# Optimization experiments

Hardware: AMD Instinct MI355X
Metric: run time of the kernel (lower is better)

Reference implementation:

```python
import jax, jax.numpy as jnp
import numpy as np

V, K, C, F = 100000, 64, 3, 16
HID = [64, 64, 64]  # 'large' pca-net hidden widths (config.yaml stand-in)
EPS = 1e-4


def setup_inputs() -> dict:
    key = jax.random.key(0)
    ks = jax.random.split(key, 12)
    inp = {
        "coordinates": jax.random.normal(ks[0], (V, C), jnp.float32),
        "distsq": jax.random.uniform(ks[1], (V, K), jnp.float32),
        "features": jax.random.uniform(ks[2], (V, F), jnp.float32),
        "n_idxs": jax.random.randint(ks[3], (V, K), 0, V, jnp.int32),
    }
    dims = [C * C] + HID + [C * C]
    for i in range(len(dims) - 1):
        fan_in = dims[i]
        inp[f"W{i}"] = jax.random.normal(ks[4 + 2 * i], (dims[i], dims[i + 1]), jnp.float32) / np.sqrt(fan_in)
        inp[f"b{i}"] = jnp.zeros((dims[i + 1],), jnp.float32)
    return inp


def _neighbour_covariance(coordinates, distsq, features, n_idxs):
    # gather neighbour coords/features: [V,K,C], [V,K,F]
    nbc = jnp.take(coordinates, n_idxs, axis=0)
    nbf = jnp.take(features, n_idxs, axis=0)
    # per-neighbour per-feature weights, distsq pre-scaled by 10 in call()
    w = nbf * jnp.exp(-10.0 * distsq)[:, :, None]          # [V,K,F]
    wsum = jnp.sum(w, axis=1) + EPS                         # [V,F]
    mean = jnp.einsum("vkf,vkc->vfc", w, nbc) / wsum[:, :, None]  # [V,F,C]
    # E[x x^T] - mu mu^T (avoids materializing [V,K,F,C] centered diffs)
    m2 = jnp.einsum("vkf,vkc,vkd->vfcd", w, nbc, nbc) / wsum[:, :, None, None]
    cov = m2 - mean[:, :, :, None] * mean[:, :, None, :]    # [V,F,C,C]
    return cov, mean


def reference(coordinates, distsq, features, n_idxs,
              W0, b0, W1, b1, W2, b2, W3, b3):
    cov, mean = _neighbour_covariance(coordinates, distsq, features, n_idxs)
    x = cov.reshape(-1, C * C)                              # [V*F, C^2]
    # per-layer path: ELU on every layer, including the final one
    for Wl, bl in ((W0, b0), (W1, b1), (W2, b2), (W3, b3)):
        x = jax.nn.elu(x @ Wl + bl)
    return x.reshape(-1, F * C * C)                         # [V, F*C^2]
```

## Files before the change

kernel.cpp:

```cpp
#include <hip/hip_runtime.h>
#include <math.h>

#define NV 100000
#define NK 64
#define NF 16
#define EPS_W 1e-4f
#define WS_NEED ((size_t)NV * 16 * 32)

typedef __attribute__((ext_vector_type(8))) short bf16x8;
typedef __attribute__((ext_vector_type(4))) float f32x4;

__device__ __forceinline__ unsigned int f2bfu(float x) {
    union { float f; unsigned int u; } a; a.f = x;
    return (a.u + 0x7FFFu + ((a.u >> 16) & 1u)) >> 16;
}
__device__ __forceinline__ unsigned int packbf(float lo, float hi) {
    return f2bfu(lo) | (f2bfu(hi) << 16);
}
__device__ __forceinline__ float eluf(float x) {
    return x > 0.f ? x : __expf(x) - 1.f;
}

__launch_bounds__(256)
__global__ void cov_kernel(const float* __restrict__ coords,
                           const float* __restrict__ distsq,
                           const float* __restrict__ feats,
                           const int*   __restrict__ nidx,
                           unsigned char* __restrict__ ws)
{
    __shared__ float sEW[16][64];
    __shared__ int   sIX[16][64];
    const int tid = threadIdx.x;
    const int gv  = tid >> 4;
    const int f   = tid & 15;
    const int v   = blockIdx.x * 16 + gv;

    {
        const size_t base = (size_t)v * NK + 4 * f;
        float4 d4 = *(const float4*)(distsq + base);
        int4   i4 = *(const int4*)(nidx + base);
        sEW[gv][4*f+0] = __expf(-10.f * d4.x);
        sEW[gv][4*f+1] = __expf(-10.f * d4.y);
        sEW[gv][4*f+2] = __expf(-10.f * d4.z);
        sEW[gv][4*f+3] = __expf(-10.f * d4.w);
        sIX[gv][4*f+0] = i4.x; sIX[gv][4*f+1] = i4.y;
        sIX[gv][4*f+2] = i4.z; sIX[gv][4*f+3] = i4.w;
    }
    __syncthreads();

    float s = 0.f, m0=0.f,m1=0.f,m2=0.f;
    float q00=0.f,q01=0.f,q02=0.f,q11=0.f,q12=0.f,q22=0.f;

    #pragma unroll 4
    for (int k = 0; k < NK; ++k) {
        int   idx = sIX[gv][k];
        float ew  = sEW[gv][k];
        float w   = feats[(size_t)idx * NF + f] * ew;
        float x = coords[(size_t)idx*3+0];
        float y = coords[(size_t)idx*3+1];
        float z = coords[(size_t)idx*3+2];
        s += w;
        m0 = fmaf(w,x,m0); m1 = fmaf(w,y,m1); m2 = fmaf(w,z,m2);
        float wx=w*x, wy=w*y, wz=w*z;
        q00=fmaf(wx,x,q00); q01=fmaf(wx,y,q01); q02=fmaf(wx,z,q02);
        q11=fmaf(wy,y,q11); q12=fmaf(wy,z,q12); q22=fmaf(wz,z,q22);
    }
    float inv = 1.f / (s + EPS_W);
    float mu0=m0*inv, mu1=m1*inv, mu2=m2*inv;
    float c00=fmaf(-mu0,mu0,q00*inv);
    float c01=fmaf(-mu0,mu1,q01*inv);
    float c02=fmaf(-mu0,mu2,q02*inv);
    float c11=fmaf(-mu1,mu1,q11*inv);
    float c12=fmaf(-mu1,mu2,q12*inv);
    float c22=fmaf(-mu2,mu2,q22*inv);

    uint4 lo, hi;
    lo.x = packbf(c00, c01);
    lo.y = packbf(c02, c01);
    lo.z = packbf(c11, c12);
    lo.w = packbf(c02, c12);
    hi.x = packbf(c22, 1.0f);
    hi.y = 0u; hi.z = 0u; hi.w = 0u;

    uint4* dst = (uint4*)(ws + ((size_t)v * 16 + f) * 32);
    dst[0] = lo;
    dst[1] = hi;
}

__device__ __forceinline__ bf16x8 rdfrag(const short* hb, int c, int g, int kc) {
    int boff = ((kc << 6) + (g << 4)) ^ ((c & 7) << 4);
    return *(const bf16x8*)(hb + c * 64 + (boff >> 1));
}
__device__ __forceinline__ void wrH(short* hb, int c, int g, int t,
                                    unsigned int p01, unsigned int p23) {
    int boff = ((t << 5) + (g << 3)) ^ ((c & 7) << 4);
    uint2 val; val.x = p01; val.y = p23;
    *(uint2*)(hb + c * 64 + (boff >> 1)) = val;
}

__launch_bounds__(256, 2)
__global__ void mlp_kernel(const unsigned char* __restrict__ ws,
                           const float* __restrict__ W0, const float* __restrict__ b0,
                           const float* __restrict__ W1, const float* __restrict__ b1,
                           const float* __restrict__ W2, const float* __restrict__ b2,
                           const float* __restrict__ W3, const float* __restrict__ b3,
                           float* __restrict__ out)
{
    __shared__ __align__(16) short hbuf[4][16 * 64];
    const int tid  = threadIdx.x;
    const int wid  = tid >> 6;
    const int lane = tid & 63;
    const int c    = lane & 15;
    const int g    = lane >> 4;
    short* hb = &hbuf[wid][0];

    union U8 { short s[8]; bf16x8 v; };

    bf16x8 w0f[4], w1f[8], w2f[8], w3f[2];
    #pragma unroll
    for (int t = 0; t < 4; ++t) {
        U8 u;
        #pragma unroll
        for (int i = 0; i < 8; ++i) {
            int k = 8 * g + i;
            float val = 0.f;
            if (k < 9)       val = W0[k * 64 + 16 * t + c];
            else if (k == 9) val = b0[16 * t + c];
            u.s[i] = (short)f2bfu(val);
        }
        w0f[t] = u.v;
    }
    #pragma unroll
    for (int t = 0; t < 4; ++t) {
        #pragma unroll
        for (int kc = 0; kc < 2; ++kc) {
            U8 u1, u2;
            #pragma unroll
            for (int i = 0; i < 8; ++i) {
                int k = 32 * kc + 8 * g + i;
                u1.s[i] = (short)f2bfu(W1[k * 64 + 16 * t + c]);
                u2.s[i] = (short)f2bfu(W2[k * 64 + 16 * t + c]);
            }
            w1f[2 * t + kc] = u1.v;
            w2f[2 * t + kc] = u2.v;
        }
    }
    #pragma unroll
    for (int kc = 0; kc < 2; ++kc) {
        U8 u;
        #pragma unroll
        for (int i = 0; i < 8; ++i) {
            int k = 32 * kc + 8 * g + i;
            u.s[i] = (short)f2bfu(c < 9 ? W3[k * 9 + c] : 0.f);
        }
        w3f[kc] = u.v;
    }

    float b1v[16], b2v[16], b3v[4];
    #pragma unroll
    for (int t = 0; t < 4; ++t)
        #pragma unroll
        for (int r = 0; r < 4; ++r) {
            b1v[4*t+r] = b1[16*t + 4*g + r];
            b2v[4*t+r] = b2[16*t + 4*g + r];
        }
    #pragma unroll
    for (int r = 0; r < 4; ++r)
        b3v[r] = (4*g + r < 9) ? b3[4*g + r] : 0.f;

    const int stride = gridDim.x * 4;
    for (int t0 = blockIdx.x * 4 + wid; t0 < NV; t0 += stride) {
        f32x4 a[4];
        {
            union { uint4 q; bf16x8 v; } bin;
            bin.q = *(const uint4*)(ws + (size_t)t0 * 512 + (c << 5) + ((g & 1) << 4));
            #pragma unroll
            for (int t = 0; t < 4; ++t) {
                f32x4 z4 = {0.f, 0.f, 0.f, 0.f};
                a[t] = __builtin_amdgcn_mfma_f32_16x16x32_bf16(w0f[t], bin.v, z4, 0, 0, 0);
            }
            #pragma unroll
            for (int t = 0; t < 4; ++t)
                wrH(hb, c, g, t, packbf(eluf(a[t][0]), eluf(a[t][1])),
                                 packbf(eluf(a[t][2]), eluf(a[t][3])));
        }
        {
            bf16x8 h0 = rdfrag(hb, c, g, 0);
            bf16x8 h1 = rdfrag(hb, c, g, 1);
            #pragma unroll
            for (int t = 0; t < 4; ++t) {
                f32x4 acc = { b1v[4*t+0], b1v[4*t+1], b1v[4*t+2], b1v[4*t+3] };
                acc = __builtin_amdgcn_mfma_f32_16x16x32_bf16(w1f[2*t+0], h0, acc, 0, 0, 0);
                acc = __builtin_amdgcn_mfma_f32_16x16x32_bf16(w1f[2*t+1], h1, acc, 0, 0, 0);
                a[t] = acc;
            }
            #pragma unroll
            for (int t = 0; t < 4; ++t)
                wrH(hb, c, g, t, packbf(eluf(a[t][0]), eluf(a[t][1])),
                                 packbf(eluf(a[t][2]), eluf(a[t][3])));
        }
        {
            bf16x8 h0 = rdfrag(hb, c, g, 0);
            bf16x8 h1 = rdfrag(hb, c, g, 1);
            #pragma unroll
            for (int t = 0; t < 4; ++t) {
                f32x4 acc = { b2v[4*t+0], b2v[4*t+1], b2v[4*t+2], b2v[4*t+3] };
                acc = __builtin_amdgcn_mfma_f32_16x16x32_bf16(w2f[2*t+0], h0, acc, 0, 0, 0);
                acc = __builtin_amdgcn_mfma_f32_16x16x32_bf16(w2f[2*t+1], h1, acc, 0, 0, 0);
                a[t] = acc;
            }
            #pragma unroll
            for (int t = 0; t < 4; ++t)
                wrH(hb, c, g, t, packbf(eluf(a[t][0]), eluf(a[t][1])),
                                 packbf(eluf(a[t][2]), eluf(a[t][3])));
        }
        {
            bf16x8 h0 = rdfrag(hb, c, g, 0);
            bf16x8 h1 = rdfrag(hb, c, g, 1);
            f32x4 acc = { b3v[0], b3v[1], b3v[2], b3v[3] };
            acc = __builtin_amdgcn_mfma_f32_16x16x32_bf16(w3f[0], h0, acc, 0, 0, 0);
            acc = __builtin_amdgcn_mfma_f32_16x16x32_bf16(w3f[1], h1, acc, 0, 0, 0);
            float* op = out + (size_t)(t0 * 16 + c) * 9 + (g << 2);
            if (g < 2) {
                op[0] = eluf(acc[0]); op[1] = eluf(acc[1]);
                op[2] = eluf(acc[2]); op[3] = eluf(acc[3]);
            } else if (g == 2) {
                op[0] = eluf(acc[0]);
            }
        }
    }
}

__launch_bounds__(256, 2)
__global__ void fused_pca_mlp(const float* __restrict__ coords,
                              const float* __restrict__ distsq,
                              const float* __restrict__ feats,
                              const int*   __restrict__ nidx,
                              const float* __restrict__ W0, const float* __restrict__ b0,
                              const float* __restrict__ W1, const float* __restrict__ b1,
                              const float* __restrict__ W2, const float* __restrict__ b2,
                              const float* __restrict__ W3, const float* __restrict__ b3,
                              float* __restrict__ out)
{
    __shared__ __align__(16) float sW0t[64 * 9];
    __shared__ __align__(16) float sW1t[64 * 64];
    __shared__ __align__(16) float sW2t[64 * 64];
    __shared__ __align__(16) float sW3t[9 * 64];
    __shared__ float sB0[64], sB1[64], sB2[64], sB3[9];
    const int tid = threadIdx.x;
    for (int t = tid; t < 64 * 9; t += 256) { int j = t / 9, i = t - j * 9; sW0t[t] = W0[i * 64 + j]; }
    for (int t = tid; t < 64 * 64; t += 256) { int j = t >> 6, i = t & 63; sW1t[t] = W1[i * 64 + j]; }
    for (int t = tid; t < 64 * 64; t += 256) { int j = t >> 6, i = t & 63; sW2t[t] = W2[i * 64 + j]; }
    for (int t = tid; t < 9 * 64; t += 256) { int j = t >> 6, i = t & 63; sW3t[t] = W3[i * 9 + j]; }
    if (tid < 64) { sB0[tid] = b0[tid]; sB1[tid] = b1[tid]; sB2[tid] = b2[tid]; }
    if (tid < 9)  { sB3[tid] = b3[tid]; }
    __syncthreads();
    const int g = tid >> 4, f = tid & 15;
    const int v = blockIdx.x * 16 + g;
    if (v >= NV) return;
    const int* nix = nidx + (size_t)v * NK;
    const float* dsq = distsq + (size_t)v * NK;
    float s = 0.f, m0=0,m1=0,m2=0, q00=0,q01=0,q02=0,q11=0,q12=0,q22=0;
    #pragma unroll 4
    for (int k = 0; k < NK; ++k) {
        int idx = nix[k];
        float ew = __expf(-10.0f * dsq[k]);
        float w = feats[(size_t)idx * NF + f] * ew;
        float x = coords[(size_t)idx*3+0], y = coords[(size_t)idx*3+1], z = coords[(size_t)idx*3+2];
        s += w; m0 = fmaf(w,x,m0); m1 = fmaf(w,y,m1); m2 = fmaf(w,z,m2);
        float wx=w*x, wy=w*y, wz=w*z;
        q00=fmaf(wx,x,q00); q01=fmaf(wx,y,q01); q02=fmaf(wx,z,q02);
        q11=fmaf(wy,y,q11); q12=fmaf(wy,z,q12); q22=fmaf(wz,z,q22);
    }
    float inv = 1.0f/(s+EPS_W), mu0=m0*inv, mu1=m1*inv, mu2=m2*inv;
    float xr[9];
    xr[0]=fmaf(-mu0,mu0,q00*inv); xr[1]=fmaf(-mu0,mu1,q01*inv); xr[2]=fmaf(-mu0,mu2,q02*inv);
    xr[3]=xr[1]; xr[4]=fmaf(-mu1,mu1,q11*inv); xr[5]=fmaf(-mu1,mu2,q12*inv);
    xr[6]=xr[2]; xr[7]=xr[5]; xr[8]=fmaf(-mu2,mu2,q22*inv);
    float h[64], gg[64];
    #pragma unroll
    for (int j = 0; j < 64; ++j) {
        float aa = sB0[j]; const float* wr = sW0t + j * 9;
        #pragma unroll
        for (int i = 0; i < 9; ++i) aa = fmaf(xr[i], wr[i], aa);
        h[j] = eluf(aa);
    }
    #pragma unroll
    for (int j = 0; j < 64; ++j) {
        float aa = sB1[j]; const float4* wr = (const float4*)(sW1t + (j << 6));
        #pragma unroll
        for (int i4 = 0; i4 < 16; ++i4) { float4 wv = wr[i4];
            aa = fmaf(h[4*i4+0],wv.x,aa); aa = fmaf(h[4*i4+1],wv.y,aa);
            aa = fmaf(h[4*i4+2],wv.z,aa); aa = fmaf(h[4*i4+3],wv.w,aa); }
        gg[j] = eluf(aa);
    }
    #pragma unroll
    for (int j = 0; j < 64; ++j) {
        float aa = sB2[j]; const float4* wr = (const float4*)(sW2t + (j << 6));
        #pragma unroll
        for (int i4 = 0; i4 < 16; ++i4) { float4 wv = wr[i4];
            aa = fmaf(gg[4*i4+0],wv.x,aa); aa = fmaf(gg[4*i4+1],wv.y,aa);
            aa = fmaf(gg[4*i4+2],wv.z,aa); aa = fmaf(gg[4*i4+3],wv.w,aa); }
        h[j] = eluf(aa);
    }
    float o[9];
    #pragma unroll
    for (int j = 0; j < 9; ++j) {
        float aa = sB3[j]; const float4* wr = (const float4*)(sW3t + (j << 6));
        #pragma unroll
        for (int i4 = 0; i4 < 16; ++i4) { float4 wv = wr[i4];
            aa = fmaf(h[4*i4+0],wv.x,aa); aa = fmaf(h[4*i4+1],wv.y,aa);
            aa = fmaf(h[4*i4+2],wv.z,aa); aa = fmaf(h[4*i4+3],wv.w,aa); }
        o[j] = eluf(aa);
    }
    float* op = out + ((size_t)v * NF + f) * 9;
    #pragma unroll
    for (int j = 0; j < 9; ++j) op[j] = o[j];
}

extern "C" void kernel_launch(void* const* d_in, const int* in_sizes, int n_in,
                              void* d_out, int out_size, void* d_ws, size_t ws_size,
                              hipStream_t stream) {
    (void)in_sizes; (void)n_in; (void)out_size;
    const float* coords = (const float*)d_in[0];
    const float* distsq = (const float*)d_in[1];
    const float* feats  = (const float*)d_in[2];
    const int*   nidx   = (const int*)d_in[3];
    const float* W0 = (const float*)d_in[4];
    const float* b0 = (const float*)d_in[5];
    const float* W1 = (const float*)d_in[6];
    const float* b1 = (const float*)d_in[7];
    const float* W2 = (const float*)d_in[8];
    const float* b2 = (const float*)d_in[9];
    const float* W3 = (const float*)d_in[10];
    const float* b3 = (const float*)d_in[11];
    float* out = (float*)d_out;

    if (ws_size >= WS_NEED) {
        unsigned char* ws = (unsigned char*)d_ws;
        hipLaunchKernelGGL(cov_kernel, dim3(NV / 16), dim3(256), 0, stream,
                           coords, distsq, feats, nidx, ws);
        hipLaunchKernelGGL(mlp_kernel, dim3(1024), dim3(256), 0, stream,
                           ws, W0, b0, W1, b1, W2, b2, W3, b3, out);
    } else {
        hipLaunchKernelGGL(fused_pca_mlp, dim3(NV / 16), dim3(256), 0, stream,
                           coords, distsq, feats, nidx,
                           W0, b0, W1, b1, W2, b2, W3, b3, out);
    }
}
```

Before: 209.8 us.

## Fuse covariance gather and MFMA MLP into one persistent per-wave kernel

```diff
diff --git a/kernel.cpp b/kernel.cpp
--- a/kernel.cpp
+++ b/kernel.cpp
@@ -5,86 +5,20 @@
 #define NK 64
 #define NF 16
 #define EPS_W 1e-4f
-#define WS_NEED ((size_t)NV * 16 * 32)
+#define NGRP (NV / 4)
+#define GRID 625
 
 typedef __attribute__((ext_vector_type(8))) short bf16x8;
 typedef __attribute__((ext_vector_type(4))) float f32x4;
 
-__device__ __forceinline__ unsigned int f2bfu(float x) {
-    union { float f; unsigned int u; } a; a.f = x;
-    return (a.u + 0x7FFFu + ((a.u >> 16) & 1u)) >> 16;
-}
-__device__ __forceinline__ unsigned int packbf(float lo, float hi) {
-    return f2bfu(lo) | (f2bfu(hi) << 16);
+__device__ __forceinline__ unsigned short bfu(float x) {
+    return __builtin_bit_cast(unsigned short, (__bf16)x);
+}
+__device__ __forceinline__ unsigned int pk2(float lo, float hi) {
+    return (unsigned int)bfu(lo) | ((unsigned int)bfu(hi) << 16);
 }
 __device__ __forceinline__ float eluf(float x) {
     return x > 0.f ? x : __expf(x) - 1.f;
-}
-
-__launch_bounds__(256)
-__global__ void cov_kernel(const float* __restrict__ coords,
-                           const float* __restrict__ distsq,
-                           const float* __restrict__ feats,
-                           const int*   __restrict__ nidx,
-                           unsigned char* __restrict__ ws)
-{
-    __shared__ float sEW[16][64];
-    __shared__ int   sIX[16][64];
-    const int tid = threadIdx.x;
-    const int gv  = tid >> 4;
-    const int f   = tid & 15;
-    const int v   = blockIdx.x * 16 + gv;
-
-    {
-        const size_t base = (size_t)v * NK + 4 * f;
-        float4 d4 = *(const float4*)(distsq + base);
-        int4   i4 = *(const int4*)(nidx + base);
-        sEW[gv][4*f+0] = __expf(-10.f * d4.x);
-        sEW[gv][4*f+1] = __expf(-10.f * d4.y);
-        sEW[gv][4*f+2] = __expf(-10.f * d4.z);
-        sEW[gv][4*f+3] = __expf(-10.f * d4.w);
-        sIX[gv][4*f+0] = i4.x; sIX[gv][4*f+1] = i4.y;
-        sIX[gv][4*f+2] = i4.z; sIX[gv][4*f+3] = i4.w;
-    }
-    __syncthreads();
-
-    float s = 0.f, m0=0.f,m1=0.f,m2=0.f;
-    float q00=0.f,q01=0.f,q02=0.f,q11=0.f,q12=0.f,q22=0.f;
-
-    #pragma unroll 4
-    for (int k = 0; k < NK; ++k) {
-        int   idx = sIX[gv][k];
-        float ew  = sEW[gv][k];
-        float w   = feats[(size_t)idx * NF + f] * ew;
-        float x = coords[(size_t)idx*3+0];
-        float y = coords[(size_t)idx*3+1];
-        float z = coords[(size_t)idx*3+2];
-        s += w;
-        m0 = fmaf(w,x,m0); m1 = fmaf(w,y,m1); m2 = fmaf(w,z,m2);
-        float wx=w*x, wy=w*y, wz=w*z;
-        q00=fmaf(wx,x,q00); q01=fmaf(wx,y,q01); q02=fmaf(wx,z,q02);
-        q11=fmaf(wy,y,q11); q12=fmaf(wy,z,q12); q22=fmaf(wz,z,q22);
-    }
-    float inv = 1.f / (s + EPS_W);
-    float mu0=m0*inv, mu1=m1*inv, mu2=m2*inv;
-    float c00=fmaf(-mu0,mu0,q00*inv);
-    float c01=fmaf(-mu0,mu1,q01*inv);
-    float c02=fmaf(-mu0,mu2,q02*inv);
-    float c11=fmaf(-mu1,mu1,q11*inv);
-    float c12=fmaf(-mu1,mu2,q12*inv);
-    float c22=fmaf(-mu2,mu2,q22*inv);
-
-    uint4 lo, hi;
-    lo.x = packbf(c00, c01);
-    lo.y = packbf(c02, c01);
-    lo.z = packbf(c11, c12);
-    lo.w = packbf(c02, c12);
-    hi.x = packbf(c22, 1.0f);
-    hi.y = 0u; hi.z = 0u; hi.w = 0u;
-
-    uint4* dst = (uint4*)(ws + ((size_t)v * 16 + f) * 32);
-    dst[0] = lo;
-    dst[1] = hi;
 }
 
 __device__ __forceinline__ bf16x8 rdfrag(const short* hb, int c, int g, int kc) {
@@ -98,21 +32,29 @@
     *(uint2*)(hb + c * 64 + (boff >> 1)) = val;
 }
 
-__launch_bounds__(256, 2)
-__global__ void mlp_kernel(const unsigned char* __restrict__ ws,
-                           const float* __restrict__ W0, const float* __restrict__ b0,
-                           const float* __restrict__ W1, const float* __restrict__ b1,
-                           const float* __restrict__ W2, const float* __restrict__ b2,
-                           const float* __restrict__ W3, const float* __restrict__ b3,
-                           float* __restrict__ out)
+__launch_bounds__(256, 3)
+__global__ void fused_kernel(const float* __restrict__ coords,
+                             const float* __restrict__ distsq,
+                             const float* __restrict__ feats,
+                             const int*   __restrict__ nidx,
+                             const float* __restrict__ W0, const float* __restrict__ b0,
+                             const float* __restrict__ W1, const float* __restrict__ b1,
+                             const float* __restrict__ W2, const float* __restrict__ b2,
+                             const float* __restrict__ W3, const float* __restrict__ b3,
+                             float* __restrict__ out)
 {
+    __shared__ float sEW[4][4][64];
+    __shared__ int   sIX[4][4][64];
+    __shared__ __align__(16) short rowbuf[4][64 * 24];
     __shared__ __align__(16) short hbuf[4][16 * 64];
+
     const int tid  = threadIdx.x;
     const int wid  = tid >> 6;
     const int lane = tid & 63;
-    const int c    = lane & 15;
-    const int g    = lane >> 4;
+    const int c = lane & 15;
+    const int g = lane >> 4;
     short* hb = &hbuf[wid][0];
+    short* rb = &rowbuf[wid][0];
 
     union U8 { short s[8]; bf16x8 v; };
 
@@ -126,7 +68,7 @@
             float val = 0.f;
             if (k < 9)       val = W0[k * 64 + 16 * t + c];
             else if (k == 9) val = b0[16 * t + c];
-            u.s[i] = (short)f2bfu(val);
+            u.s[i] = (short)bfu(val);
         }
         w0f[t] = u.v;
     }
@@ -138,8 +80,8 @@
             #pragma unroll
             for (int i = 0; i < 8; ++i) {
                 int k = 32 * kc + 8 * g + i;
-                u1.s[i] = (short)f2bfu(W1[k * 64 + 16 * t + c]);
-                u2.s[i] = (short)f2bfu(W2[k * 64 + 16 * t + c]);
+                u1.s[i] = (short)bfu(W1[k * 64 + 16 * t + c]);
+                u2.s[i] = (short)bfu(W2[k * 64 + 16 * t + c]);
             }
             w1f[2 * t + kc] = u1.v;
             w2f[2 * t + kc] = u2.v;
@@ -151,7 +93,7 @@
         #pragma unroll
         for (int i = 0; i < 8; ++i) {
             int k = 32 * kc + 8 * g + i;
-            u.s[i] = (short)f2bfu(c < 9 ? W3[k * 9 + c] : 0.f);
+            u.s[i] = (short)bfu(c < 9 ? W3[k * 9 + c] : 0.f);
         }
         w3f[kc] = u.v;
     }
@@ -161,167 +103,136 @@
     for (int t = 0; t < 4; ++t)
         #pragma unroll
         for (int r = 0; r < 4; ++r) {
-            b1v[4*t+r] = b1[16*t + 4*g + r];
-            b2v[4*t+r] = b2[16*t + 4*g + r];
+            b1v[4 * t + r] = b1[16 * t + 4 * g + r];
+            b2v[4 * t + r] = b2[16 * t + 4 * g + r];
         }
     #pragma unroll
     for (int r = 0; r < 4; ++r)
-        b3v[r] = (4*g + r < 9) ? b3[4*g + r] : 0.f;
-
-    const int stride = gridDim.x * 4;
-    for (int t0 = blockIdx.x * 4 + wid; t0 < NV; t0 += stride) {
-        f32x4 a[4];
+        b3v[r] = (4 * g + r < 9) ? b3[4 * g + r] : 0.f;
+
+    for (int grp = blockIdx.x * 4 + wid; grp < NGRP; grp += GRID * 4) {
+        const int v = grp * 4 + g;
+
         {
-            union { uint4 q; bf16x8 v; } bin;
-            bin.q = *(const uint4*)(ws + (size_t)t0 * 512 + (c << 5) + ((g & 1) << 4));
-            #pragma unroll
-            for (int t = 0; t < 4; ++t) {
-                f32x4 z4 = {0.f, 0.f, 0.f, 0.f};
-                a[t] = __builtin_amdgcn_mfma_f32_16x16x32_bf16(w0f[t], bin.v, z4, 0, 0, 0);
-            }
-            #pragma unroll
-            for (int t = 0; t < 4; ++t)
-                wrH(hb, c, g, t, packbf(eluf(a[t][0]), eluf(a[t][1])),
-                                 packbf(eluf(a[t][2]), eluf(a[t][3])));
-        }
+            const size_t base = (size_t)v * NK + 4 * c;
+            float4 d4 = *(const float4*)(distsq + base);
+            int4   i4 = *(const int4*)(nidx + base);
+            sEW[wid][g][4 * c + 0] = __expf(-10.f * d4.x);
+            sEW[wid][g][4 * c + 1] = __expf(-10.f * d4.y);
+            sEW[wid][g][4 * c + 2] = __expf(-10.f * d4.z);
+            sEW[wid][g][4 * c + 3] = __expf(-10.f * d4.w);
+            sIX[wid][g][4 * c + 0] = i4.x; sIX[wid][g][4 * c + 1] = i4.y;
+            sIX[wid][g][4 * c + 2] = i4.z; sIX[wid][g][4 * c + 3] = i4.w;
+        }
+        __asm__ volatile("s_waitcnt lgkmcnt(0)" ::: "memory");
+
+        float s = 0.f, m0 = 0.f, m1 = 0.f, m2 = 0.f;
+        float q00 = 0.f, q01 = 0.f, q02 = 0.f, q11 = 0.f, q12 = 0.f, q22 = 0.f;
+        #pragma unroll 4
+        for (int k = 0; k < NK; ++k) {
+            int   idx = sIX[wid][g][k];
+            float ew  = sEW[wid][g][k];
+            float w   = feats[(size_t)idx * NF + c] * ew;
+            float x = coords[(size_t)idx * 3 + 0];
+            float y = coords[(size_t)idx * 3 + 1];
+            float z = coords[(size_t)idx * 3 + 2];
+            s += w;
+            m0 = fmaf(w, x, m0); m1 = fmaf(w, y, m1); m2 = fmaf(w, z, m2);
+            float wx = w * x, wy = w * y, wz = w * z;
+            q00 = fmaf(wx, x, q00); q01 = fmaf(wx, y, q01); q02 = fmaf(wx, z, q02);
+            q11 = fmaf(wy, y, q11); q12 = fmaf(wy, z, q12);
+            q22 = fmaf(wz, z, q22);
+        }
+        float inv = 1.f / (s + EPS_W);
+        float mu0 = m0 * inv, mu1 = m1 * inv, mu2 = m2 * inv;
+        float c00 = fmaf(-mu0, mu0, q00 * inv);
+        float c01 = fmaf(-mu0, mu1, q01 * inv);
+        float c02 = fmaf(-mu0, mu2, q02 * inv);
+        float c11 = fmaf(-mu1, mu1, q11 * inv);
+        float c12 = fmaf(-mu1, mu2, q12 * inv);
+        float c22 = fmaf(-mu2, mu2, q22 * inv);
+
         {
-            bf16x8 h0 = rdfrag(hb, c, g, 0);
-            bf16x8 h1 = rdfrag(hb, c, g, 1);
-            #pragma unroll
-            for (int t = 0; t < 4; ++t) {
-                f32x4 acc = { b1v[4*t+0], b1v[4*t+1], b1v[4*t+2], b1v[4*t+3] };
-                acc = __builtin_amdgcn_mfma_f32_16x16x32_bf16(w1f[2*t+0], h0, acc, 0, 0, 0);
-                acc = __builtin_amdgcn_mfma_f32_16x16x32_bf16(w1f[2*t+1], h1, acc, 0, 0, 0);
-                a[t] = acc;
-            }
-            #pragma unroll
-            for (int t = 0; t < 4; ++t)
-                wrH(hb, c, g, t, packbf(eluf(a[t][0]), eluf(a[t][1])),
-                                 packbf(eluf(a[t][2]), eluf(a[t][3])));
-        }
-        {
-            bf16x8 h0 = rdfrag(hb, c, g, 0);
-            bf16x8 h1 = rdfrag(hb, c, g, 1);
-            #pragma unroll
-            for (int t = 0; t < 4; ++t) {
-                f32x4 acc = { b2v[4*t+0], b2v[4*t+1], b2v[4*t+2], b2v[4*t+3] };
-                acc = __builtin_amdgcn_mfma_f32_16x16x32_bf16(w2f[2*t+0], h0, acc, 0, 0, 0);
-                acc = __builtin_amdgcn_mfma_f32_16x16x32_bf16(w2f[2*t+1], h1, acc, 0, 0, 0);
-                a[t] = acc;
-            }
-            #pragma unroll
-            for (int t = 0; t < 4; ++t)
-                wrH(hb, c, g, t, packbf(eluf(a[t][0]), eluf(a[t][1])),
-                                 packbf(eluf(a[t][2]), eluf(a[t][3])));
-        }
-        {
-            bf16x8 h0 = rdfrag(hb, c, g, 0);
-            bf16x8 h1 = rdfrag(hb, c, g, 1);
-            f32x4 acc = { b3v[0], b3v[1], b3v[2], b3v[3] };
-            acc = __builtin_amdgcn_mfma_f32_16x16x32_bf16(w3f[0], h0, acc, 0, 0, 0);
-            acc = __builtin_amdgcn_mfma_f32_16x16x32_bf16(w3f[1], h1, acc, 0, 0, 0);
-            float* op = out + (size_t)(t0 * 16 + c) * 9 + (g << 2);
-            if (g < 2) {
-                op[0] = eluf(acc[0]); op[1] = eluf(acc[1]);
-                op[2] = eluf(acc[2]); op[3] = eluf(acc[3]);
-            } else if (g == 2) {
-                op[0] = eluf(acc[0]);
-            }
-        }
-    }
-}
-
-__launch_bounds__(256, 2)
-__global__ void fused_pca_mlp(const float* __restrict__ coords,
-                              const float* __restrict__ distsq,
-                              const float* __restrict__ feats,
-                              const int*   __restrict__ nidx,
-                              const float* __restrict__ W0, const float* __restrict__ b0,
-                              const float* __restrict__ W1, const float* __restrict__ b1,
-                              const float* __restrict__ W2, const float* __restrict__ b2,
-                              const float* __restrict__ W3, const float* __restrict__ b3,
-                              float* __restrict__ out)
-{
-    __shared__ __align__(16) float sW0t[64 * 9];
-    __shared__ __align__(16) float sW1t[64 * 64];
-    __shared__ __align__(16) float sW2t[64 * 64];
-    __shared__ __align__(16) float sW3t[9 * 64];
-    __shared__ float sB0[64], sB1[64], sB2[64], sB3[9];
-    const int tid = threadIdx.x;
-    for (int t = tid; t < 64 * 9; t += 256) { int j = t / 9, i = t - j * 9; sW0t[t] = W0[i * 64 + j]; }
-    for (int t = tid; t < 64 * 64; t += 256) { int j = t >> 6, i = t & 63; sW1t[t] = W1[i * 64 + j]; }
-    for (int t = tid; t < 64 * 64; t += 256) { int j = t >> 6, i = t & 63; sW2t[t] = W2[i * 64 + j]; }
-    for (int t = tid; t < 9 * 64; t += 256) { int j = t >> 6, i = t & 63; sW3t[t] = W3[i * 9 + j]; }
-    if (tid < 64) { sB0[tid] = b0[tid]; sB1[tid] = b1[tid]; sB2[tid] = b2[tid]; }
-    if (tid < 9)  { sB3[tid] = b3[tid]; }
-    __syncthreads();
-    const int g = tid >> 4, f = tid & 15;
-    const int v = blockIdx.x * 16 + g;
-    if (v >= NV) return;
-    const int* nix = nidx + (size_t)v * NK;
-    const float* dsq = distsq + (size_t)v * NK;
-    float s = 0.f, m0=0,m1=0,m2=0, q00=0,q01=0,q02=0,q11=0,q12=0,q22=0;
-    #pragma unroll 4
-    for (int k = 0; k < NK; ++k) {
-        int idx = nix[k];
-        float ew = __expf(-10.0f * dsq[k]);
-        float w = feats[(size_t)idx * NF + f] * ew;
-        float x = coords[(size_t)idx*3+0], y = coords[(size_t)idx*3+1], z = coords[(size_t)idx*3+2];
-        s += w; m0 = fmaf(w,x,m0); m1 = fmaf(w,y,m1); m2 = fmaf(w,z,m2);
-        float wx=w*x, wy=w*y, wz=w*z;
-        q00=fmaf(wx,x,q00); q01=fmaf(wx,y,q01); q02=fmaf(wx,z,q02);
-        q11=fmaf(wy,y,q11); q12=fmaf(wy,z,q12); q22=fmaf(wz,z,q22);
-    }
-    float inv = 1.0f/(s+EPS_W), mu0=m0*inv, mu1=m1*inv, mu2=m2*inv;
-    float xr[9];
-    xr[0]=fmaf(-mu0,mu0,q00*inv); xr[1]=fmaf(-mu0,mu1,q01*inv); xr[2]=fmaf(-mu0,mu2,q02*inv);
-    xr[3]=xr[1]; xr[4]=fmaf(-mu1,mu1,q11*inv); xr[5]=fmaf(-mu1,mu2,q12*inv);
-    xr[6]=xr[2]; xr[7]=xr[5]; xr[8]=fmaf(-mu2,mu2,q22*inv);
-    float h[64], gg[64];
-    #pragma unroll
-    for (int j = 0; j < 64; ++j) {
-        float aa = sB0[j]; const float* wr = sW0t + j * 9;
-        #pragma unroll
-        for (int i = 0; i < 9; ++i) aa = fmaf(xr[i], wr[i], aa);
-        h[j] = eluf(aa);
-    }
-    #pragma unroll
-    for (int j = 0; j < 64; ++j) {
-        float aa = sB1[j]; const float4* wr = (const float4*)(sW1t + (j << 6));
-        #pragma unroll
-        for (int i4 = 0; i4 < 16; ++i4) { float4 wv = wr[i4];
-            aa = fmaf(h[4*i4+0],wv.x,aa); aa = fmaf(h[4*i4+1],wv.y,aa);
-            aa = fmaf(h[4*i4+2],wv.z,aa); aa = fmaf(h[4*i4+3],wv.w,aa); }
-        gg[j] = eluf(aa);
-    }
-    #pragma unroll
-    for (int j = 0; j < 64; ++j) {
-        float aa = sB2[j]; const float4* wr = (const float4*)(sW2t + (j << 6));
-        #pragma unroll
-        for (int i4 = 0; i4 < 16; ++i4) { float4 wv = wr[i4];
-            aa = fmaf(gg[4*i4+0],wv.x,aa); aa = fmaf(gg[4*i4+1],wv.y,aa);
-            aa = fmaf(gg[4*i4+2],wv.z,aa); aa = fmaf(gg[4*i4+3],wv.w,aa); }
-        h[j] = eluf(aa);
-    }
-    float o[9];
-    #pragma unroll
-    for (int j = 0; j < 9; ++j) {
-        float aa = sB3[j]; const float4* wr = (const float4*)(sW3t + (j << 6));
-        #pragma unroll
-        for (int i4 = 0; i4 < 16; ++i4) { float4 wv = wr[i4];
-            aa = fmaf(h[4*i4+0],wv.x,aa); aa = fmaf(h[4*i4+1],wv.y,aa);
-            aa = fmaf(h[4*i4+2],wv.z,aa); aa = fmaf(h[4*i4+3],wv.w,aa); }
-        o[j] = eluf(aa);
-    }
-    float* op = out + ((size_t)v * NF + f) * 9;
-    #pragma unroll
-    for (int j = 0; j < 9; ++j) op[j] = o[j];
+            uint4 lo, hi;
+            lo.x = pk2(c00, c01);
+            lo.y = pk2(c02, c01);
+            lo.z = pk2(c11, c12);
+            lo.w = pk2(c02, c12);
+            hi.x = pk2(c22, 1.0f);
+            hi.y = 0u; hi.z = 0u; hi.w = 0u;
+            uint4* dst = (uint4*)(rb + lane * 24);
+            dst[0] = lo;
+            dst[1] = hi;
+        }
+        __asm__ volatile("s_waitcnt lgkmcnt(0)" ::: "memory");
+
+        #pragma unroll 1
+        for (int vv = 0; vv < 4; ++vv) {
+            f32x4 a[4];
+            {
+                bf16x8 bin = *(const bf16x8*)(rb + (16 * vv + c) * 24 + ((g & 1) << 3));
+                #pragma unroll
+                for (int t = 0; t < 4; ++t) {
+                    f32x4 z4 = {0.f, 0.f, 0.f, 0.f};
+                    a[t] = __builtin_amdgcn_mfma_f32_16x16x32_bf16(w0f[t], bin, z4, 0, 0, 0);
+                }
+                #pragma unroll
+                for (int t = 0; t < 4; ++t)
+                    wrH(hb, c, g, t, pk2(eluf(a[t][0]), eluf(a[t][1])),
+                                     pk2(eluf(a[t][2]), eluf(a[t][3])));
+            }
+            {
+                bf16x8 h0 = rdfrag(hb, c, g, 0);
+                bf16x8 h1 = rdfrag(hb, c, g, 1);
+                #pragma unroll
+                for (int t = 0; t < 4; ++t) {
+                    f32x4 acc = { b1v[4*t+0], b1v[4*t+1], b1v[4*t+2], b1v[4*t+3] };
+                    acc = __builtin_amdgcn_mfma_f32_16x16x32_bf16(w1f[2*t+0], h0, acc, 0, 0, 0);
+                    acc = __builtin_amdgcn_mfma_f32_16x16x32_bf16(w1f[2*t+1], h1, acc, 0, 0, 0);
+                    a[t] = acc;
+                }
+                #pragma unroll
+                for (int t = 0; t < 4; ++t)
+                    wrH(hb, c, g, t, pk2(eluf(a[t][0]), eluf(a[t][1])),
+                                     pk2(eluf(a[t][2]), eluf(a[t][3])));
+            }
+            {
+                bf16x8 h0 = rdfrag(hb, c, g, 0);
+                bf16x8 h1 = rdfrag(hb, c, g, 1);
+                #pragma unroll
+                for (int t = 0; t < 4; ++t) {
+                    f32x4 acc = { b2v[4*t+0], b2v[4*t+1], b2v[4*t+2], b2v[4*t+3] };
+                    acc = __builtin_amdgcn_mfma_f32_16x16x32_bf16(w2f[2*t+0], h0, acc, 0, 0, 0);
+                    acc = __builtin_amdgcn_mfma_f32_16x16x32_bf16(w2f[2*t+1], h1, acc, 0, 0, 0);
+                    a[t] = acc;
+                }
+                #pragma unroll
+                for (int t = 0; t < 4; ++t)
+                    wrH(hb, c, g, t, pk2(eluf(a[t][0]), eluf(a[t][1])),
+                                     pk2(eluf(a[t][2]), eluf(a[t][3])));
+            }
+            {
+                bf16x8 h0 = rdfrag(hb, c, g, 0);
+                bf16x8 h1 = rdfrag(hb, c, g, 1);
+                f32x4 acc = { b3v[0], b3v[1], b3v[2], b3v[3] };
+                acc = __builtin_amdgcn_mfma_f32_16x16x32_bf16(w3f[0], h0, acc, 0, 0, 0);
+                acc = __builtin_amdgcn_mfma_f32_16x16x32_bf16(w3f[1], h1, acc, 0, 0, 0);
+                float* op = out + (size_t)((grp * 4 + vv) * 16 + c) * 9 + (g << 2);
+                if (g < 2) {
+                    op[0] = eluf(acc[0]); op[1] = eluf(acc[1]);
+                    op[2] = eluf(acc[2]); op[3] = eluf(acc[3]);
+                } else if (g == 2) {
+                    op[0] = eluf(acc[0]);
+                }
+            }
+        }
+    }
 }
 
 extern "C" void kernel_launch(void* const* d_in, const int* in_sizes, int n_in,
                               void* d_out, int out_size, void* d_ws, size_t ws_size,
                               hipStream_t stream) {
-    (void)in_sizes; (void)n_in; (void)out_size;
+    (void)in_sizes; (void)n_in; (void)out_size; (void)d_ws; (void)ws_size;
     const float* coords = (const float*)d_in[0];
     const float* distsq = (const float*)d_in[1];
     const float* feats  = (const float*)d_in[2];
@@ -336,15 +247,7 @@
     const float* b3 = (const float*)d_in[11];
     float* out = (float*)d_out;
 
-    if (ws_size >= WS_NEED) {
-        unsigned char* ws = (unsigned char*)d_ws;
-        hipLaunchKernelGGL(cov_kernel, dim3(NV / 16), dim3(256), 0, stream,
-                           coords, distsq, feats, nidx, ws);
-        hipLaunchKernelGGL(mlp_kernel, dim3(1024), dim3(256), 0, stream,
-                           ws, W0, b0, W1, b1, W2, b2, W3, b3, out);
-    } else {
-        hipLaunchKernelGGL(fused_pca_mlp, dim3(NV / 16), dim3(256), 0, stream,
-                           coords, distsq, feats, nidx,
-                           W0, b0, W1, b1, W2, b2, W3, b3, out);
-    }
-}
+    hipLaunchKernelGGL(fused_kernel, dim3(GRID), dim3(256), 0, stream,
+                       coords, distsq, feats, nidx,
+                       W0, b0, W1, b1, W2, b2, W3, b3, out);
+}
```

After: 341.5 us. 62.8% more time.

## Precompute per-neighbour coordinate moments in shared memory, reducing covariance to feature dot products

Applied to the files above, without the earlier changes.

```diff
diff --git a/kernel.cpp b/kernel.cpp
--- a/kernel.cpp
+++ b/kernel.cpp
@@ -6,80 +6,87 @@
 #define NF 16
 #define EPS_W 1e-4f
 #define WS_NEED ((size_t)NV * 16 * 32)
+#define ZSTRIDE 776
 
 typedef __attribute__((ext_vector_type(8))) short bf16x8;
 typedef __attribute__((ext_vector_type(4))) float f32x4;
 
-__device__ __forceinline__ unsigned int f2bfu(float x) {
-    union { float f; unsigned int u; } a; a.f = x;
-    return (a.u + 0x7FFFu + ((a.u >> 16) & 1u)) >> 16;
-}
-__device__ __forceinline__ unsigned int packbf(float lo, float hi) {
-    return f2bfu(lo) | (f2bfu(hi) << 16);
+__device__ __forceinline__ unsigned short bfu(float x) {
+    return __builtin_bit_cast(unsigned short, (__bf16)x);
+}
+__device__ __forceinline__ unsigned int pk2(float lo, float hi) {
+    return (unsigned int)bfu(lo) | ((unsigned int)bfu(hi) << 16);
 }
 __device__ __forceinline__ float eluf(float x) {
     return x > 0.f ? x : __expf(x) - 1.f;
 }
 
 __launch_bounds__(256)
-__global__ void cov_kernel(const float* __restrict__ coords,
-                           const float* __restrict__ distsq,
-                           const float* __restrict__ feats,
-                           const int*   __restrict__ nidx,
-                           unsigned char* __restrict__ ws)
+__global__ void cov2_kernel(const float* __restrict__ coords,
+                            const float* __restrict__ distsq,
+                            const float* __restrict__ feats,
+                            const int*   __restrict__ nidx,
+                            unsigned char* __restrict__ ws)
 {
-    __shared__ float sEW[16][64];
-    __shared__ int   sIX[16][64];
+    __shared__ __align__(16) float sZ[16 * ZSTRIDE];
+
     const int tid = threadIdx.x;
-    const int gv  = tid >> 4;
-    const int f   = tid & 15;
-    const int v   = blockIdx.x * 16 + gv;
-
-    {
-        const size_t base = (size_t)v * NK + 4 * f;
-        float4 d4 = *(const float4*)(distsq + base);
-        int4   i4 = *(const int4*)(nidx + base);
-        sEW[gv][4*f+0] = __expf(-10.f * d4.x);
-        sEW[gv][4*f+1] = __expf(-10.f * d4.y);
-        sEW[gv][4*f+2] = __expf(-10.f * d4.z);
-        sEW[gv][4*f+3] = __expf(-10.f * d4.w);
-        sIX[gv][4*f+0] = i4.x; sIX[gv][4*f+1] = i4.y;
-        sIX[gv][4*f+2] = i4.z; sIX[gv][4*f+3] = i4.w;
+
+    #pragma unroll
+    for (int r = 0; r < 4; ++r) {
+        int t  = tid + r * 256;
+        int gv = t >> 6, k = t & 63;
+        int v  = blockIdx.x * 16 + gv;
+        float d  = distsq[(size_t)v * NK + k];
+        int  idx = nidx[(size_t)v * NK + k];
+        float ew = __expf(-10.f * d);
+        const float* cp = coords + (size_t)idx * 3;
+        float x = cp[0], y = cp[1], z = cp[2];
+        float* zr = sZ + gv * ZSTRIDE + k * 12;
+        float4 z0 = { ew * x * x, ew * x * y, ew * x * z, ew * y * y };
+        float4 z1 = { ew * y * z, ew * z * z, ew * x,     ew * y     };
+        float4 z2 = { ew * z,     ew,         __int_as_float(idx), 0.f };
+        *(float4*)(zr + 0) = z0;
+        *(float4*)(zr + 4) = z1;
+        *(float4*)(zr + 8) = z2;
     }
     __syncthreads();
 
-    float s = 0.f, m0=0.f,m1=0.f,m2=0.f;
-    float q00=0.f,q01=0.f,q02=0.f,q11=0.f,q12=0.f,q22=0.f;
+    const int gv = tid >> 4, f = tid & 15;
+    const int v  = blockIdx.x * 16 + gv;
+    const float* zb = sZ + gv * ZSTRIDE;
+
+    float a0=0.f,a1=0.f,a2=0.f,a3=0.f,a4=0.f,a5=0.f,a6=0.f,a7=0.f,a8=0.f,a9=0.f;
 
     #pragma unroll 4
     for (int k = 0; k < NK; ++k) {
-        int   idx = sIX[gv][k];
-        float ew  = sEW[gv][k];
-        float w   = feats[(size_t)idx * NF + f] * ew;
-        float x = coords[(size_t)idx*3+0];
-        float y = coords[(size_t)idx*3+1];
-        float z = coords[(size_t)idx*3+2];
-        s += w;
-        m0 = fmaf(w,x,m0); m1 = fmaf(w,y,m1); m2 = fmaf(w,z,m2);
-        float wx=w*x, wy=w*y, wz=w*z;
-        q00=fmaf(wx,x,q00); q01=fmaf(wx,y,q01); q02=fmaf(wx,z,q02);
-        q11=fmaf(wy,y,q11); q12=fmaf(wy,z,q12); q22=fmaf(wz,z,q22);
-    }
-    float inv = 1.f / (s + EPS_W);
-    float mu0=m0*inv, mu1=m1*inv, mu2=m2*inv;
-    float c00=fmaf(-mu0,mu0,q00*inv);
-    float c01=fmaf(-mu0,mu1,q01*inv);
-    float c02=fmaf(-mu0,mu2,q02*inv);
-    float c11=fmaf(-mu1,mu1,q11*inv);
-    float c12=fmaf(-mu1,mu2,q12*inv);
-    float c22=fmaf(-mu2,mu2,q22*inv);
+        float4 z0 = *(const float4*)(zb + k * 12 + 0);
+        float4 z1 = *(const float4*)(zb + k * 12 + 4);
+        float4 z2 = *(const float4*)(zb + k * 12 + 8);
+        int   idx = __float_as_int(z2.z);
+        float ft  = feats[(size_t)idx * NF + f];
+        a0 = fmaf(ft, z0.x, a0); a1 = fmaf(ft, z0.y, a1);
+        a2 = fmaf(ft, z0.z, a2); a3 = fmaf(ft, z0.w, a3);
+        a4 = fmaf(ft, z1.x, a4); a5 = fmaf(ft, z1.y, a5);
+        a6 = fmaf(ft, z1.z, a6); a7 = fmaf(ft, z1.w, a7);
+        a8 = fmaf(ft, z2.x, a8); a9 = fmaf(ft, z2.y, a9);
+    }
+
+    float inv = 1.f / (a9 + EPS_W);
+    float mu0 = a6 * inv, mu1 = a7 * inv, mu2 = a8 * inv;
+    float c00 = fmaf(-mu0, mu0, a0 * inv);
+    float c01 = fmaf(-mu0, mu1, a1 * inv);
+    float c02 = fmaf(-mu0, mu2, a2 * inv);
+    float c11 = fmaf(-mu1, mu1, a3 * inv);
+    float c12 = fmaf(-mu1, mu2, a4 * inv);
+    float c22 = fmaf(-mu2, mu2, a5 * inv);
 
     uint4 lo, hi;
-    lo.x = packbf(c00, c01);
-    lo.y = packbf(c02, c01);
-    lo.z = packbf(c11, c12);
-    lo.w = packbf(c02, c12);
-    hi.x = packbf(c22, 1.0f);
+    lo.x = pk2(c00, c01);
+    lo.y = pk2(c02, c01);
+    lo.z = pk2(c11, c12);
+    lo.w = pk2(c02, c12);
+    hi.x = pk2(c22, 1.0f);
     hi.y = 0u; hi.z = 0u; hi.w = 0u;
 
     uint4* dst = (uint4*)(ws + ((size_t)v * 16 + f) * 32);
@@ -126,7 +133,7 @@
             float val = 0.f;
             if (k < 9)       val = W0[k * 64 + 16 * t + c];
             else if (k == 9) val = b0[16 * t + c];
-            u.s[i] = (short)f2bfu(val);
+            u.s[i] = (short)bfu(val);
         }
         w0f[t] = u.v;
     }
@@ -138,8 +145,8 @@
             #pragma unroll
             for (int i = 0; i < 8; ++i) {
                 int k = 32 * kc + 8 * g + i;
-                u1.s[i] = (short)f2bfu(W1[k * 64 + 16 * t + c]);
-                u2.s[i] = (short)f2bfu(W2[k * 64 + 16 * t + c]);
+                u1.s[i] = (short)bfu(W1[k * 64 + 16 * t + c]);
+                u2.s[i] = (short)bfu(W2[k * 64 + 16 * t + c]);
             }
             w1f[2 * t + kc] = u1.v;
             w2f[2 * t + kc] = u2.v;
@@ -151,7 +158,7 @@
         #pragma unroll
         for (int i = 0; i < 8; ++i) {
             int k = 32 * kc + 8 * g + i;
-            u.s[i] = (short)f2bfu(c < 9 ? W3[k * 9 + c] : 0.f);
+            u.s[i] = (short)bfu(c < 9 ? W3[k * 9 + c] : 0.f);
         }
         w3f[kc] = u.v;
     }
@@ -161,12 +168,12 @@
     for (int t = 0; t < 4; ++t)
         #pragma unroll
         for (int r = 0; r < 4; ++r) {
-            b1v[4*t+r] = b1[16*t + 4*g + r];
-            b2v[4*t+r] = b2[16*t + 4*g + r];
+            b1v[4 * t + r] = b1[16 * t + 4 * g + r];
+            b2v[4 * t + r] = b2[16 * t + 4 * g + r];
         }
     #pragma unroll
     for (int r = 0; r < 4; ++r)
-        b3v[r] = (4*g + r < 9) ? b3[4*g + r] : 0.f;
+        b3v[r] = (4 * g + r < 9) ? b3[4 * g + r] : 0.f;
 
     const int stride = gridDim.x * 4;
     for (int t0 = blockIdx.x * 4 + wid; t0 < NV; t0 += stride) {
@@ -181,8 +188,8 @@
             }
             #pragma unroll
             for (int t = 0; t < 4; ++t)
-                wrH(hb, c, g, t, packbf(eluf(a[t][0]), eluf(a[t][1])),
-                                 packbf(eluf(a[t][2]), eluf(a[t][3])));
+                wrH(hb, c, g, t, pk2(eluf(a[t][0]), eluf(a[t][1])),
+                                 pk2(eluf(a[t][2]), eluf(a[t][3])));
         }
         {
             bf16x8 h0 = rdfrag(hb, c, g, 0);
@@ -196,8 +203,8 @@
             }
             #pragma unroll
             for (int t = 0; t < 4; ++t)
-                wrH(hb, c, g, t, packbf(eluf(a[t][0]), eluf(a[t][1])),
-                                 packbf(eluf(a[t][2]), eluf(a[t][3])));
+                wrH(hb, c, g, t, pk2(eluf(a[t][0]), eluf(a[t][1])),
+                                 pk2(eluf(a[t][2]), eluf(a[t][3])));
         }
         {
             bf16x8 h0 = rdfrag(hb, c, g, 0);
@@ -211,8 +218,8 @@
             }
             #pragma unroll
             for (int t = 0; t < 4; ++t)
-                wrH(hb, c, g, t, packbf(eluf(a[t][0]), eluf(a[t][1])),
-                                 packbf(eluf(a[t][2]), eluf(a[t][3])));
+                wrH(hb, c, g, t, pk2(eluf(a[t][0]), eluf(a[t][1])),
+                                 pk2(eluf(a[t][2]), eluf(a[t][3])));
         }
         {
             bf16x8 h0 = rdfrag(hb, c, g, 0);
@@ -338,9 +345,9 @@
 
     if (ws_size >= WS_NEED) {
         unsigned char* ws = (unsigned char*)d_ws;
-        hipLaunchKernelGGL(cov_kernel, dim3(NV / 16), dim3(256), 0, stream,
+        hipLaunchKernelGGL(cov2_kernel, dim3(NV / 16), dim3(256), 0, stream,
                            coords, distsq, feats, nidx, ws);
-        hipLaunchKernelGGL(mlp_kernel, dim3(1024), dim3(256), 0, stream,
+        hipLaunchKernelGGL(mlp_kernel, dim3(2048), dim3(256), 0, stream,
                            ws, W0, b0, W1, b1, W2, b2, W3, b3, out);
     } else {
         hipLaunchKernelGGL(fused_pca_mlp, dim3(NV / 16), dim3(256), 0, stream,
```

Measured after the change: 236.9 us. +13.0%, slower.
